# Kernel optimization log

Measured on AMD Instinct MI355X. Metric: run time of the kernel, lower is better.

Reference implementation:

```python
import jax, jax.numpy as jnp
import numpy as np

LAYERS = [3, 256, 256, 256, 256, 256, 256, 3]
W_BC, W_DIV, W_JXB = 1.0, 1.0, 1.0  # weight1 = [1.0, 1.0, 1.0]


def setup_inputs() -> dict:
    key = jax.random.key(0)
    ks = jax.random.split(key, 32)
    N0, NF = 16384, 32768
    inp = {
        "x0": jax.random.uniform(ks[0], (N0, 1), jnp.float32),
        "y0": jax.random.uniform(ks[1], (N0, 1), jnp.float32),
        "bx0": jax.random.normal(ks[2], (N0, 1), jnp.float32),
        "by0": jax.random.normal(ks[3], (N0, 1), jnp.float32),
        "bz0": jax.random.normal(ks[4], (N0, 1), jnp.float32),
        "xyz_f": jax.random.uniform(ks[5], (NF, 3), jnp.float32),
        "lb": jnp.zeros((3,), jnp.float32),
        "ub": jnp.ones((3,), jnp.float32),
    }
    # Xavier-normal weights, zero biases (as in initialize_NN)
    for l in range(len(LAYERS) - 1):
        fan_in, fan_out = LAYERS[l], LAYERS[l + 1]
        std = (2.0 / (fan_in + fan_out)) ** 0.5
        inp[f"W{l}"] = std * jax.random.normal(ks[6 + l], (fan_in, fan_out), jnp.float32)
        inp[f"b{l}"] = jnp.zeros((1, fan_out), jnp.float32)
    return inp


def reference(x0, y0, bx0, by0, bz0, xyz_f, lb, ub,
              W0, b0, W1, b1, W2, b2, W3, b3, W4, b4, W5, b5, W6, b6):
    Ws = [W0, W1, W2, W3, W4, W5, W6]
    bs = [b0, b1, b2, b3, b4, b5, b6]

    def net(p):  # p: (3,) -> (3,) field [bx, by, bz]
        h = 2.0 * (p - lb) / (ub - lb) - 1.0
        for W, b in zip(Ws[:-1], bs[:-1]):
            h = jnp.tanh(h @ W + b[0])
        return h @ Ws[-1] + bs[-1][0]

    # Boundary term at z = 0
    pts0 = jnp.concatenate([x0, y0, jnp.zeros_like(x0)], axis=1)  # (N0, 3)
    b_bc = jax.vmap(net)(pts0)  # (N0, 3)

    # One fused forward-mode pass gives the full 3x3 Jacobian + primal,
    # replacing the 9 separate autograd.grad sweeps of the torch code.
    def val_and_jac(p):
        primal, jac = jax.vmap(lambda t: jax.jvp(net, (p,), (t,)))(jnp.eye(3, dtype=p.dtype))
        return primal[0], jac  # jac[j, i] = d b_i / d x_j

    bf, jac = jax.vmap(val_and_jac)(xyz_f)  # (NF, 3), (NF, 3, 3)

    div = jac[:, 0, 0] + jac[:, 1, 1] + jac[:, 2, 2]  # bx_x + by_y + bz_z
    bx, by, bz = bf[:, 0], bf[:, 1], bf[:, 2]
    jx = jac[:, 1, 2] - jac[:, 2, 1]  # bz_y - by_z
    jy = jac[:, 2, 0] - jac[:, 0, 2]  # bx_z - bz_x
    jz = jac[:, 0, 1] - jac[:, 1, 0]  # by_x - bx_y
    jxb = (jy * bz - jz * by) ** 2 + (jz * bx - jx * bz) ** 2 + (jx * by - jy * bx) ** 2

    loss = (W_BC * jnp.mean((b_bc[:, 0:1] - bx0) ** 2)
            + W_BC * jnp.mean((b_bc[:, 1:2] - by0) ** 2)
            + W_BC * jnp.mean((b_bc[:, 2:3] - bz0) ** 2)
            + W_DIV * jnp.mean(div ** 2)
            + W_JXB * jnp.mean(jxb))
    return loss
```

## Files before the change

kernel.cpp:

```cpp
#include <hip/hip_runtime.h>
#include <math.h>

typedef short bf16x8 __attribute__((ext_vector_type(8)));
typedef float f32x4 __attribute__((ext_vector_type(4)));

#define NPT0 16384
#define NPTF 32768

__device__ __forceinline__ short f2b(float f) {
  union { float f; unsigned u; } v; v.f = f;
  return (short)((v.u + 0x7FFFu + ((v.u >> 16) & 1u)) >> 16);
}
__device__ __forceinline__ int cvtpk(float a, float b) {
  int r;
  asm("v_cvt_pk_bf16_f32 %0, %1, %2" : "=v"(r) : "v"(a), "v"(b));
  return r;
}
__device__ __forceinline__ float tanh_fast(float z) {
  const float e = __expf(2.f * z);
  return 1.f - 2.f * __builtin_amdgcn_rcpf(e + 1.f);
}
__device__ __forceinline__ int inplane(int n, int c) {
  return ((n >> 5) << 9) + ((((n >> 3) & 3) * 16 + c) << 3) + (n & 7);
}

__global__ void prep_kernel(const float* __restrict__ W1, const float* __restrict__ W2,
                            const float* __restrict__ W3, const float* __restrict__ W4,
                            const float* __restrict__ W5, const float* __restrict__ W6,
                            short* __restrict__ Wt)
{
  const int i = blockIdx.x * 256 + threadIdx.x;
  if (i < 5 * 65536) {
    const int layer = i >> 16;
    const float* src = layer == 0 ? W1 : layer == 1 ? W2 : layer == 2 ? W3
                     : layer == 3 ? W4 : W5;
    const int w  = i & 65535;
    const int nt = w >> 12;
    const int ks = (w >> 9) & 7;
    const int l  = (w >> 3) & 63;
    const int e  = w & 7;
    const int n  = nt * 16 + (l & 15);
    const int k  = ks * 32 + (l >> 4) * 8 + e;
    Wt[i] = f2b(src[k * 256 + n]);
  } else {
    const int w  = i - 5 * 65536;
    const int ks = w >> 9;
    const int l  = (w >> 3) & 63;
    const int e  = w & 7;
    const int n  = l & 15;
    const int k  = ks * 32 + (l >> 4) * 8 + e;
    Wt[i] = (n < 3) ? f2b(W6[k * 3 + n]) : (short)0;
  }
}

__global__ __launch_bounds__(512, 4) void field_kernel(
    const float* __restrict__ xyz_f,
    const float* __restrict__ lb, const float* __restrict__ ub,
    const float* __restrict__ W0, const float* __restrict__ b0,
    const float* __restrict__ b1, const float* __restrict__ b2,
    const float* __restrict__ b3, const float* __restrict__ b4,
    const float* __restrict__ b5,
    const short* __restrict__ Wt,
    const float* __restrict__ b6,
    float* __restrict__ part_div2, float* __restrict__ part_jxb)
{
  __shared__ short act[4 * 8192];
  __shared__ float redD[4 * 96];
  const int tid = threadIdx.x;
  const int lane = tid & 63;
  const int wv = tid >> 6;
  const int c = lane & 15;
  const int kg = lane >> 4;
  const int set = wv & 3;
  const int grp = wv >> 2;

  const float lbx = lb[0], lby = lb[1], lbz = lb[2];
  const float sx = 2.f / (ub[0] - lbx);
  const float sy = 2.f / (ub[1] - lby);
  const float sz = 2.f / (ub[2] - lbz);

  {
    const int pp = tid & 15;
    const int pg = (tid >> 4) & 1;
    const int pt = blockIdx.x * 32 + pg * 16 + pp;
    const int n0 = (tid >> 5) * 16;
    const float hx = (xyz_f[pt * 3 + 0] - lbx) * sx - 1.f;
    const float hy = (xyz_f[pt * 3 + 1] - lby) * sy - 1.f;
    const float hz = (xyz_f[pt * 3 + 2] - lbz) * sz - 1.f;
    float th[16], vx[16], vy[16], vz[16];
#pragma unroll
    for (int j = 0; j < 16; ++j) {
      const int n = n0 + j;
      const float w0 = W0[n], w1 = W0[256 + n], w2 = W0[512 + n];
      const float z = b0[n] + hx * w0 + hy * w1 + hz * w2;
      const float t = tanh_fast(z);
      const float g = 1.f - t * t;
      th[j] = t;
      vx[j] = g * sx * w0;
      vy[j] = g * sy * w1;
      vz[j] = g * sz * w2;
    }
    const int ks0 = n0 >> 5;
    const int kgb = (n0 >> 3) & 3;
#pragma unroll
    for (int half = 0; half < 2; ++half) {
      const int j0 = half * 8;
      const int idx = pg * 4096 + ks0 * 512 + ((kgb + half) * 16 + pp) * 8;
      int4 o0, o1, o2, o3;
      o0.x = cvtpk(th[j0+0], th[j0+1]); o0.y = cvtpk(th[j0+2], th[j0+3]);
      o0.z = cvtpk(th[j0+4], th[j0+5]); o0.w = cvtpk(th[j0+6], th[j0+7]);
      o1.x = cvtpk(vx[j0+0], vx[j0+1]); o1.y = cvtpk(vx[j0+2], vx[j0+3]);
      o1.z = cvtpk(vx[j0+4], vx[j0+5]); o1.w = cvtpk(vx[j0+6], vx[j0+7]);
      o2.x = cvtpk(vy[j0+0], vy[j0+1]); o2.y = cvtpk(vy[j0+2], vy[j0+3]);
      o2.z = cvtpk(vy[j0+4], vy[j0+5]); o2.w = cvtpk(vy[j0+6], vy[j0+7]);
      o3.x = cvtpk(vz[j0+0], vz[j0+1]); o3.y = cvtpk(vz[j0+2], vz[j0+3]);
      o3.z = cvtpk(vz[j0+4], vz[j0+5]); o3.w = cvtpk(vz[j0+6], vz[j0+7]);
      *(int4*)&act[idx]          = o0;
      *(int4*)&act[8192 + idx]   = o1;
      *(int4*)&act[16384 + idx]  = o2;
      *(int4*)&act[24576 + idx]  = o3;
    }
  }
  __syncthreads();

  const float* const bsArr[5] = {b1, b2, b3, b4, b5};

#pragma unroll
  for (int layer = 0; layer < 5; ++layer) {
    const short* wbase = Wt + layer * 65536 + (set * 4) * 4096 + lane * 8;

    f32x4 acc[4][4];
#pragma unroll
    for (int t = 0; t < 4; ++t)
#pragma unroll
      for (int s = 0; s < 4; ++s) acc[t][s] = (f32x4){0.f, 0.f, 0.f, 0.f};

#pragma unroll
    for (int ks = 0; ks < 8; ++ks) {
      const int sa = grp * 4096 + ks * 512 + lane * 8;
      const bf16x8 a0 = *(const bf16x8*)&act[sa];
      const bf16x8 a1 = *(const bf16x8*)&act[8192 + sa];
      const bf16x8 a2 = *(const bf16x8*)&act[16384 + sa];
      const bf16x8 a3 = *(const bf16x8*)&act[24576 + sa];
#pragma unroll
      for (int t = 0; t < 4; ++t) {
        const bf16x8 w = *(const bf16x8*)(wbase + t * 4096 + ks * 512);
        acc[t][0] = __builtin_amdgcn_mfma_f32_16x16x32_bf16(w, a0, acc[t][0], 0, 0, 0);
        acc[t][1] = __builtin_amdgcn_mfma_f32_16x16x32_bf16(w, a1, acc[t][1], 0, 0, 0);
        acc[t][2] = __builtin_amdgcn_mfma_f32_16x16x32_bf16(w, a2, acc[t][2], 0, 0, 0);
        acc[t][3] = __builtin_amdgcn_mfma_f32_16x16x32_bf16(w, a3, acc[t][3], 0, 0, 0);
      }
    }
    __syncthreads();

    const float* bl = bsArr[layer];
#pragma unroll
    for (int t = 0; t < 4; ++t) {
      const int n0 = (set * 4 + t) * 16 + kg * 4;
      const f32x4 bias = *(const f32x4*)(bl + n0);
      float th[4], gd[4];
#pragma unroll
      for (int r = 0; r < 4; ++r) {
        th[r] = tanh_fast(acc[t][0][r] + bias[r]);
        gd[r] = 1.f - th[r] * th[r];
      }
      int2 o0, o1, o2, o3;
      o0.x = cvtpk(th[0], th[1]);
      o0.y = cvtpk(th[2], th[3]);
      o1.x = cvtpk(gd[0] * acc[t][1][0], gd[1] * acc[t][1][1]);
      o1.y = cvtpk(gd[2] * acc[t][1][2], gd[3] * acc[t][1][3]);
      o2.x = cvtpk(gd[0] * acc[t][2][0], gd[1] * acc[t][2][1]);
      o2.y = cvtpk(gd[2] * acc[t][2][2], gd[3] * acc[t][2][3]);
      o3.x = cvtpk(gd[0] * acc[t][3][0], gd[1] * acc[t][3][1]);
      o3.y = cvtpk(gd[2] * acc[t][3][2], gd[3] * acc[t][3][3]);
      const int idx = grp * 4096 + inplane(n0, c);
      *(int2*)&act[idx]          = o0;
      *(int2*)&act[8192 + idx]   = o1;
      *(int2*)&act[16384 + idx]  = o2;
      *(int2*)&act[24576 + idx]  = o3;
    }
    __syncthreads();
  }

  {
    const int s = wv >> 1, g = wv & 1;
    const short* w6 = Wt + 5 * 65536 + lane * 8;
    f32x4 accT = (f32x4){0.f, 0.f, 0.f, 0.f};
#pragma unroll
    for (int ks = 0; ks < 8; ++ks) {
      const bf16x8 w = *(const bf16x8*)(w6 + ks * 512);
      const bf16x8 b = *(const bf16x8*)&act[s * 8192 + g * 4096 + ks * 512 + lane * 8];
      accT = __builtin_amdgcn_mfma_f32_16x16x32_bf16(w, b, accT, 0, 0, 0);
    }
    if (kg == 0) {
      redD[s * 96 + 0  + g * 16 + c] = accT[0];
      redD[s * 96 + 32 + g * 16 + c] = accT[1];
      redD[s * 96 + 64 + g * 16 + c] = accT[2];
    }
  }
  __syncthreads();
  if (tid < 32) {
    const int p = tid;
    const float bx = redD[0 + p]   + b6[0];
    const float by = redD[32 + p]  + b6[1];
    const float bz = redD[64 + p]  + b6[2];
    const float j00 = redD[96 + p],  j01 = redD[128 + p], j02 = redD[160 + p];
    const float j10 = redD[192 + p], j11 = redD[224 + p], j12 = redD[256 + p];
    const float j20 = redD[288 + p], j21 = redD[320 + p], j22 = redD[352 + p];
    const float dv = j00 + j11 + j22;
    const float jx = j12 - j21;
    const float jy = j20 - j02;
    const float jz = j01 - j10;
    const float e1 = jy * bz - jz * by;
    const float e2 = jz * bx - jx * bz;
    const float e3 = jx * by - jy * bx;
    float d2 = dv * dv;
    float jb = e1 * e1 + e2 * e2 + e3 * e3;
#pragma unroll
    for (int m = 1; m < 32; m <<= 1) {
      d2 += __shfl_xor(d2, m);
      jb += __shfl_xor(jb, m);
    }
    if (tid == 0) {
      part_div2[blockIdx.x] = d2;
      part_jxb[blockIdx.x]  = jb;
    }
  }
}

__global__ __launch_bounds__(512, 4) void bc_kernel(
    const float* __restrict__ x0, const float* __restrict__ y0,
    const float* __restrict__ bx0, const float* __restrict__ by0,
    const float* __restrict__ bz0,
    const float* __restrict__ lb, const float* __restrict__ ub,
    const float* __restrict__ W0, const float* __restrict__ b0,
    const float* __restrict__ b1, const float* __restrict__ b2,
    const float* __restrict__ b3, const float* __restrict__ b4,
    const float* __restrict__ b5,
    const short* __restrict__ Wt,
    const float* __restrict__ b6,
    float* __restrict__ part_bc)
{
  __shared__ short act[8192];
  __shared__ float red[2];
  const int tid = threadIdx.x;
  const int lane = tid & 63;
  const int wv = tid >> 6;
  const int c = lane & 15;
  const int kg = lane >> 4;

  const float lbx = lb[0], lby = lb[1], lbz = lb[2];
  const float sx = 2.f / (ub[0] - lbx);
  const float sy = 2.f / (ub[1] - lby);
  const float sz = 2.f / (ub[2] - lbz);

  {
    const int pp = tid & 15;
    const int pg = (tid >> 4) & 1;
    const int pt = blockIdx.x * 32 + pg * 16 + pp;
    const int n0 = (tid >> 5) * 16;
    const float hx = (x0[pt] - lbx) * sx - 1.f;
    const float hy = (y0[pt] - lby) * sy - 1.f;
    const float hz = (0.f - lbz) * sz - 1.f;
    float th[16];
#pragma unroll
    for (int j = 0; j < 16; ++j) {
      const int n = n0 + j;
      const float z = b0[n] + hx * W0[n] + hy * W0[256 + n] + hz * W0[512 + n];
      th[j] = tanh_fast(z);
    }
    const int ks0 = n0 >> 5;
    const int kgb = (n0 >> 3) & 3;
#pragma unroll
    for (int half = 0; half < 2; ++half) {
      const int j0 = half * 8;
      int4 o;
      o.x = cvtpk(th[j0+0], th[j0+1]); o.y = cvtpk(th[j0+2], th[j0+3]);
      o.z = cvtpk(th[j0+4], th[j0+5]); o.w = cvtpk(th[j0+6], th[j0+7]);
      *(int4*)&act[pg * 4096 + ks0 * 512 + ((kgb + half) * 16 + pp) * 8] = o;
    }
  }
  __syncthreads();

  const float* const bsArr[5] = {b1, b2, b3, b4, b5};

#pragma unroll
  for (int layer = 0; layer < 5; ++layer) {
    const short* wbase = Wt + layer * 65536 + (wv * 2) * 4096 + lane * 8;

    bf16x8 a[2][8];
#pragma unroll
    for (int g = 0; g < 2; ++g)
#pragma unroll
      for (int ks = 0; ks < 8; ++ks)
        a[g][ks] = *(const bf16x8*)&act[g * 4096 + ks * 512 + lane * 8];
    __syncthreads();

    f32x4 acc[2][2];
#pragma unroll
    for (int t = 0; t < 2; ++t)
#pragma unroll
      for (int g = 0; g < 2; ++g) acc[t][g] = (f32x4){0.f, 0.f, 0.f, 0.f};

#pragma unroll
    for (int ks = 0; ks < 8; ++ks) {
      const bf16x8 w0 = *(const bf16x8*)(wbase + ks * 512);
      const bf16x8 w1 = *(const bf16x8*)(wbase + 4096 + ks * 512);
      acc[0][0] = __builtin_amdgcn_mfma_f32_16x16x32_bf16(w0, a[0][ks], acc[0][0], 0, 0, 0);
      acc[0][1] = __builtin_amdgcn_mfma_f32_16x16x32_bf16(w0, a[1][ks], acc[0][1], 0, 0, 0);
      acc[1][0] = __builtin_amdgcn_mfma_f32_16x16x32_bf16(w1, a[0][ks], acc[1][0], 0, 0, 0);
      acc[1][1] = __builtin_amdgcn_mfma_f32_16x16x32_bf16(w1, a[1][ks], acc[1][1], 0, 0, 0);
    }

    const float* bl = bsArr[layer];
#pragma unroll
    for (int t = 0; t < 2; ++t) {
      const int n0 = (wv * 2 + t) * 16 + kg * 4;
      const f32x4 bias = *(const f32x4*)(bl + n0);
#pragma unroll
      for (int g = 0; g < 2; ++g) {
        float th[4];
#pragma unroll
        for (int r = 0; r < 4; ++r) th[r] = tanh_fast(acc[t][g][r] + bias[r]);
        int2 o;
        o.x = cvtpk(th[0], th[1]);
        o.y = cvtpk(th[2], th[3]);
        *(int2*)&act[g * 4096 + inplane(n0, c)] = o;
      }
    }
    __syncthreads();
  }

  if (wv < 2) {
    const int g = wv;
    const short* w6 = Wt + 5 * 65536 + lane * 8;
    f32x4 accT = (f32x4){0.f, 0.f, 0.f, 0.f};
#pragma unroll
    for (int ks = 0; ks < 8; ++ks) {
      const bf16x8 w = *(const bf16x8*)(w6 + ks * 512);
      const bf16x8 b = *(const bf16x8*)&act[g * 4096 + ks * 512 + lane * 8];
      accT = __builtin_amdgcn_mfma_f32_16x16x32_bf16(w, b, accT, 0, 0, 0);
    }
    if (lane < 16) {
      const int pt = blockIdx.x * 32 + g * 16 + lane;
      const float ex = accT[0] + b6[0] - bx0[pt];
      const float ey = accT[1] + b6[1] - by0[pt];
      const float ez = accT[2] + b6[2] - bz0[pt];
      float abc = ex * ex + ey * ey + ez * ez;
#pragma unroll
      for (int m = 1; m < 16; m <<= 1) abc += __shfl_xor(abc, m);
      if (lane == 0) red[g] = abc;
    }
  }
  __syncthreads();
  if (tid == 0) part_bc[blockIdx.x] = red[0] + red[1];
}

__global__ void reduce_kernel(const float* __restrict__ parts, float* __restrict__ out)
{
  __shared__ float sdata[12];
  const int tid = threadIdx.x, lane = tid & 63, wv = tid >> 6;
  float d = 0.f, j = 0.f, b = 0.f;
  for (int i = tid; i < 1024; i += 256) { d += parts[i]; j += parts[1024 + i]; }
  for (int i = tid; i < 512; i += 256) b += parts[2048 + i];
  for (int off = 32; off > 0; off >>= 1) {
    d += __shfl_down(d, off);
    j += __shfl_down(j, off);
    b += __shfl_down(b, off);
  }
  if (lane == 0) {
    sdata[wv * 3 + 0] = d;
    sdata[wv * 3 + 1] = j;
    sdata[wv * 3 + 2] = b;
  }
  __syncthreads();
  if (tid == 0) {
    float sd = 0.f, sj = 0.f, sb = 0.f;
    for (int w = 0; w < 4; ++w) {
      sd += sdata[w * 3 + 0];
      sj += sdata[w * 3 + 1];
      sb += sdata[w * 3 + 2];
    }
    out[0] = sb / (float)NPT0 + sd / (float)NPTF + sj / (float)NPTF;
  }
}

extern "C" void kernel_launch(void* const* d_in, const int* in_sizes, int n_in,
                              void* d_out, int out_size, void* d_ws, size_t ws_size,
                              hipStream_t stream)
{
  const float* x0    = (const float*)d_in[0];
  const float* y0    = (const float*)d_in[1];
  const float* bx0   = (const float*)d_in[2];
  const float* by0   = (const float*)d_in[3];
  const float* bz0   = (const float*)d_in[4];
  const float* xyz_f = (const float*)d_in[5];
  const float* lb    = (const float*)d_in[6];
  const float* ub    = (const float*)d_in[7];
  const float* W0 = (const float*)d_in[8];
  const float* b0 = (const float*)d_in[9];
  const float* W1 = (const float*)d_in[10];
  const float* b1 = (const float*)d_in[11];
  const float* W2 = (const float*)d_in[12];
  const float* b2 = (const float*)d_in[13];
  const float* W3 = (const float*)d_in[14];
  const float* b3 = (const float*)d_in[15];
  const float* W4 = (const float*)d_in[16];
  const float* b4 = (const float*)d_in[17];
  const float* W5 = (const float*)d_in[18];
  const float* b5 = (const float*)d_in[19];
  const float* W6 = (const float*)d_in[20];
  const float* b6 = (const float*)d_in[21];

  short* Wt = (short*)d_ws;
  float* parts = (float*)((char*)d_ws + (5 * 65536 + 4096) * sizeof(short));
  float* p_div2 = parts;
  float* p_jxb  = parts + 1024;
  float* p_bc   = parts + 2048;

  prep_kernel<<<1296, 256, 0, stream>>>(W1, W2, W3, W4, W5, W6, Wt);
  field_kernel<<<1024, 512, 0, stream>>>(xyz_f, lb, ub, W0, b0,
      b1, b2, b3, b4, b5, Wt, b6, p_div2, p_jxb);
  bc_kernel<<<512, 512, 0, stream>>>(x0, y0, bx0, by0, bz0, lb, ub, W0, b0,
      b1, b2, b3, b4, b5, Wt, b6, p_bc);
  reduce_kernel<<<1, 256, 0, stream>>>(parts, (float*)d_out);
}
```

Baseline: 127.0 us.

## Switch MLP matmuls from 16x16x32 to 32x32x16 MFMA tiles

Replaces the 16x16x32 bf16 MFMA tiling with 32x32x16 MFMA, changing the weight pre-pack layout, the shared-memory activation layout, and the wave-to-output-column split in both the field and boundary kernels. Each wave now owns 32 output neurons across all 32 points, so it issues one weight load per k-step instead of four. The aim is fewer instructions and weight fetches per FLOP, in exchange for larger accumulator register tiles and a repacked final layer whose padding grows from 16 to 32 columns.

```diff
diff --git a/kernel.cpp b/kernel.cpp
--- a/kernel.cpp
+++ b/kernel.cpp
@@ -3,6 +3,7 @@
 
 typedef short bf16x8 __attribute__((ext_vector_type(8)));
 typedef float f32x4 __attribute__((ext_vector_type(4)));
+typedef float f32x16 __attribute__((ext_vector_type(16)));
 
 #define NPT0 16384
 #define NPTF 32768
@@ -20,8 +21,8 @@
   const float e = __expf(2.f * z);
   return 1.f - 2.f * __builtin_amdgcn_rcpf(e + 1.f);
 }
-__device__ __forceinline__ int inplane(int n, int c) {
-  return ((n >> 5) << 9) + ((((n >> 3) & 3) * 16 + c) << 3) + (n & 7);
+__device__ __forceinline__ int inplane32(int k, int p) {
+  return ((k >> 4) << 9) + (((k >> 3) & 1) << 8) + (p << 3) + (k & 7);
 }
 
 __global__ void prep_kernel(const float* __restrict__ W1, const float* __restrict__ W2,
@@ -35,20 +36,20 @@
     const float* src = layer == 0 ? W1 : layer == 1 ? W2 : layer == 2 ? W3
                      : layer == 3 ? W4 : W5;
     const int w  = i & 65535;
-    const int nt = w >> 12;
-    const int ks = (w >> 9) & 7;
+    const int nt = w >> 13;
+    const int ks = (w >> 9) & 15;
     const int l  = (w >> 3) & 63;
     const int e  = w & 7;
-    const int n  = nt * 16 + (l & 15);
-    const int k  = ks * 32 + (l >> 4) * 8 + e;
+    const int n  = nt * 32 + (l & 31);
+    const int k  = ks * 16 + (l >> 5) * 8 + e;
     Wt[i] = f2b(src[k * 256 + n]);
   } else {
     const int w  = i - 5 * 65536;
     const int ks = w >> 9;
     const int l  = (w >> 3) & 63;
     const int e  = w & 7;
-    const int n  = l & 15;
-    const int k  = ks * 32 + (l >> 4) * 8 + e;
+    const int n  = l & 31;
+    const int k  = ks * 16 + (l >> 5) * 8 + e;
     Wt[i] = (n < 3) ? f2b(W6[k * 3 + n]) : (short)0;
   }
 }
@@ -69,10 +70,8 @@
   const int tid = threadIdx.x;
   const int lane = tid & 63;
   const int wv = tid >> 6;
-  const int c = lane & 15;
-  const int kg = lane >> 4;
-  const int set = wv & 3;
-  const int grp = wv >> 2;
+  const int p = lane & 31;
+  const int h = lane >> 5;
 
   const float lbx = lb[0], lby = lb[1], lbz = lb[2];
   const float sx = 2.f / (ub[0] - lbx);
@@ -80,9 +79,8 @@
   const float sz = 2.f / (ub[2] - lbz);
 
   {
-    const int pp = tid & 15;
-    const int pg = (tid >> 4) & 1;
-    const int pt = blockIdx.x * 32 + pg * 16 + pp;
+    const int pp = tid & 31;
+    const int pt = blockIdx.x * 32 + pp;
     const int n0 = (tid >> 5) * 16;
     const float hx = (xyz_f[pt * 3 + 0] - lbx) * sx - 1.f;
     const float hy = (xyz_f[pt * 3 + 1] - lby) * sy - 1.f;
@@ -100,12 +98,11 @@
       vy[j] = g * sy * w1;
       vz[j] = g * sz * w2;
     }
-    const int ks0 = n0 >> 5;
-    const int kgb = (n0 >> 3) & 3;
+    const int idx0 = (n0 >> 4) * 512 + pp * 8;
 #pragma unroll
     for (int half = 0; half < 2; ++half) {
       const int j0 = half * 8;
-      const int idx = pg * 4096 + ks0 * 512 + ((kgb + half) * 16 + pp) * 8;
+      const int idx = idx0 + half * 256;
       int4 o0, o1, o2, o3;
       o0.x = cvtpk(th[j0+0], th[j0+1]); o0.y = cvtpk(th[j0+2], th[j0+3]);
       o0.z = cvtpk(th[j0+4], th[j0+5]); o0.w = cvtpk(th[j0+6], th[j0+7]);
@@ -127,53 +124,50 @@
 
 #pragma unroll
   for (int layer = 0; layer < 5; ++layer) {
-    const short* wbase = Wt + layer * 65536 + (set * 4) * 4096 + lane * 8;
-
-    f32x4 acc[4][4];
-#pragma unroll
-    for (int t = 0; t < 4; ++t)
-#pragma unroll
-      for (int s = 0; s < 4; ++s) acc[t][s] = (f32x4){0.f, 0.f, 0.f, 0.f};
-
-#pragma unroll
-    for (int ks = 0; ks < 8; ++ks) {
-      const int sa = grp * 4096 + ks * 512 + lane * 8;
+    const short* wbase = Wt + layer * 65536 + wv * 8192 + lane * 8;
+
+    f32x16 acc[4];
+#pragma unroll
+    for (int s = 0; s < 4; ++s)
+#pragma unroll
+      for (int r = 0; r < 16; ++r) acc[s][r] = 0.f;
+
+#pragma unroll
+    for (int ks = 0; ks < 16; ++ks) {
+      const int sa = ks * 512 + lane * 8;
       const bf16x8 a0 = *(const bf16x8*)&act[sa];
       const bf16x8 a1 = *(const bf16x8*)&act[8192 + sa];
       const bf16x8 a2 = *(const bf16x8*)&act[16384 + sa];
       const bf16x8 a3 = *(const bf16x8*)&act[24576 + sa];
-#pragma unroll
-      for (int t = 0; t < 4; ++t) {
-        const bf16x8 w = *(const bf16x8*)(wbase + t * 4096 + ks * 512);
-        acc[t][0] = __builtin_amdgcn_mfma_f32_16x16x32_bf16(w, a0, acc[t][0], 0, 0, 0);
-        acc[t][1] = __builtin_amdgcn_mfma_f32_16x16x32_bf16(w, a1, acc[t][1], 0, 0, 0);
-        acc[t][2] = __builtin_amdgcn_mfma_f32_16x16x32_bf16(w, a2, acc[t][2], 0, 0, 0);
-        acc[t][3] = __builtin_amdgcn_mfma_f32_16x16x32_bf16(w, a3, acc[t][3], 0, 0, 0);
-      }
+      const bf16x8 w = *(const bf16x8*)(wbase + ks * 512);
+      acc[0] = __builtin_amdgcn_mfma_f32_32x32x16_bf16(w, a0, acc[0], 0, 0, 0);
+      acc[1] = __builtin_amdgcn_mfma_f32_32x32x16_bf16(w, a1, acc[1], 0, 0, 0);
+      acc[2] = __builtin_amdgcn_mfma_f32_32x32x16_bf16(w, a2, acc[2], 0, 0, 0);
+      acc[3] = __builtin_amdgcn_mfma_f32_32x32x16_bf16(w, a3, acc[3], 0, 0, 0);
     }
     __syncthreads();
 
     const float* bl = bsArr[layer];
 #pragma unroll
-    for (int t = 0; t < 4; ++t) {
-      const int n0 = (set * 4 + t) * 16 + kg * 4;
+    for (int q = 0; q < 4; ++q) {
+      const int n0 = wv * 32 + q * 8 + 4 * h;
       const f32x4 bias = *(const f32x4*)(bl + n0);
       float th[4], gd[4];
 #pragma unroll
       for (int r = 0; r < 4; ++r) {
-        th[r] = tanh_fast(acc[t][0][r] + bias[r]);
+        th[r] = tanh_fast(acc[0][q * 4 + r] + bias[r]);
         gd[r] = 1.f - th[r] * th[r];
       }
       int2 o0, o1, o2, o3;
       o0.x = cvtpk(th[0], th[1]);
       o0.y = cvtpk(th[2], th[3]);
-      o1.x = cvtpk(gd[0] * acc[t][1][0], gd[1] * acc[t][1][1]);
-      o1.y = cvtpk(gd[2] * acc[t][1][2], gd[3] * acc[t][1][3]);
-      o2.x = cvtpk(gd[0] * acc[t][2][0], gd[1] * acc[t][2][1]);
-      o2.y = cvtpk(gd[2] * acc[t][2][2], gd[3] * acc[t][2][3]);
-      o3.x = cvtpk(gd[0] * acc[t][3][0], gd[1] * acc[t][3][1]);
-      o3.y = cvtpk(gd[2] * acc[t][3][2], gd[3] * acc[t][3][3]);
-      const int idx = grp * 4096 + inplane(n0, c);
+      o1.x = cvtpk(gd[0] * acc[1][q*4+0], gd[1] * acc[1][q*4+1]);
+      o1.y = cvtpk(gd[2] * acc[1][q*4+2], gd[3] * acc[1][q*4+3]);
+      o2.x = cvtpk(gd[0] * acc[2][q*4+0], gd[1] * acc[2][q*4+1]);
+      o2.y = cvtpk(gd[2] * acc[2][q*4+2], gd[3] * acc[2][q*4+3]);
+      o3.x = cvtpk(gd[0] * acc[3][q*4+0], gd[1] * acc[3][q*4+1]);
+      o3.y = cvtpk(gd[2] * acc[3][q*4+2], gd[3] * acc[3][q*4+3]);
+      const int idx = inplane32(n0 & 255, p);
       *(int2*)&act[idx]          = o0;
       *(int2*)&act[8192 + idx]   = o1;
       *(int2*)&act[16384 + idx]  = o2;
@@ -182,31 +176,32 @@
     __syncthreads();
   }
 
-  {
-    const int s = wv >> 1, g = wv & 1;
+  if (wv < 4) {
     const short* w6 = Wt + 5 * 65536 + lane * 8;
-    f32x4 accT = (f32x4){0.f, 0.f, 0.f, 0.f};
-#pragma unroll
-    for (int ks = 0; ks < 8; ++ks) {
+    f32x16 accT;
+#pragma unroll
+    for (int r = 0; r < 16; ++r) accT[r] = 0.f;
+#pragma unroll
+    for (int ks = 0; ks < 16; ++ks) {
       const bf16x8 w = *(const bf16x8*)(w6 + ks * 512);
-      const bf16x8 b = *(const bf16x8*)&act[s * 8192 + g * 4096 + ks * 512 + lane * 8];
-      accT = __builtin_amdgcn_mfma_f32_16x16x32_bf16(w, b, accT, 0, 0, 0);
-    }
-    if (kg == 0) {
-      redD[s * 96 + 0  + g * 16 + c] = accT[0];
-      redD[s * 96 + 32 + g * 16 + c] = accT[1];
-      redD[s * 96 + 64 + g * 16 + c] = accT[2];
+      const bf16x8 b = *(const bf16x8*)&act[wv * 8192 + ks * 512 + lane * 8];
+      accT = __builtin_amdgcn_mfma_f32_32x32x16_bf16(w, b, accT, 0, 0, 0);
+    }
+    if (lane < 32) {
+      redD[wv * 96 + 0  + p] = accT[0];
+      redD[wv * 96 + 32 + p] = accT[1];
+      redD[wv * 96 + 64 + p] = accT[2];
     }
   }
   __syncthreads();
   if (tid < 32) {
-    const int p = tid;
-    const float bx = redD[0 + p]   + b6[0];
-    const float by = redD[32 + p]  + b6[1];
-    const float bz = redD[64 + p]  + b6[2];
-    const float j00 = redD[96 + p],  j01 = redD[128 + p], j02 = redD[160 + p];
-    const float j10 = redD[192 + p], j11 = redD[224 + p], j12 = redD[256 + p];
-    const float j20 = redD[288 + p], j21 = redD[320 + p], j22 = redD[352 + p];
+    const int pp = tid;
+    const float bx = redD[0 + pp]   + b6[0];
+    const float by = redD[32 + pp]  + b6[1];
+    const float bz = redD[64 + pp]  + b6[2];
+    const float j00 = redD[96 + pp],  j01 = redD[128 + pp], j02 = redD[160 + pp];
+    const float j10 = redD[192 + pp], j11 = redD[224 + pp], j12 = redD[256 + pp];
+    const float j20 = redD[288 + pp], j21 = redD[320 + pp], j22 = redD[352 + pp];
     const float dv = j00 + j11 + j22;
     const float jx = j12 - j21;
     const float jy = j20 - j02;
@@ -242,12 +237,11 @@
     float* __restrict__ part_bc)
 {
   __shared__ short act[8192];
-  __shared__ float red[2];
   const int tid = threadIdx.x;
   const int lane = tid & 63;
   const int wv = tid >> 6;
-  const int c = lane & 15;
-  const int kg = lane >> 4;
+  const int p = lane & 31;
+  const int h = lane >> 5;
 
   const float lbx = lb[0], lby = lb[1], lbz = lb[2];
   const float sx = 2.f / (ub[0] - lbx);
@@ -255,9 +249,8 @@
   const float sz = 2.f / (ub[2] - lbz);
 
   {
-    const int pp = tid & 15;
-    const int pg = (tid >> 4) & 1;
-    const int pt = blockIdx.x * 32 + pg * 16 + pp;
+    const int pp = tid & 31;
+    const int pt = blockIdx.x * 32 + pp;
     const int n0 = (tid >> 5) * 16;
     const float hx = (x0[pt] - lbx) * sx - 1.f;
     const float hy = (y0[pt] - lby) * sy - 1.f;
@@ -269,15 +262,14 @@
       const float z = b0[n] + hx * W0[n] + hy * W0[256 + n] + hz * W0[512 + n];
       th[j] = tanh_fast(z);
     }
-    const int ks0 = n0 >> 5;
-    const int kgb = (n0 >> 3) & 3;
+    const int idx0 = (n0 >> 4) * 512 + pp * 8;
 #pragma unroll
     for (int half = 0; half < 2; ++half) {
       const int j0 = half * 8;
       int4 o;
       o.x = cvtpk(th[j0+0], th[j0+1]); o.y = cvtpk(th[j0+2], th[j0+3]);
       o.z = cvtpk(th[j0+4], th[j0+5]); o.w = cvtpk(th[j0+6], th[j0+7]);
-      *(int4*)&act[pg * 4096 + ks0 * 512 + ((kgb + half) * 16 + pp) * 8] = o;
+      *(int4*)&act[idx0 + half * 256] = o;
     }
   }
   __syncthreads();
@@ -286,74 +278,55 @@
 
 #pragma unroll
   for (int layer = 0; layer < 5; ++layer) {
-    const short* wbase = Wt + layer * 65536 + (wv * 2) * 4096 + lane * 8;
-
-    bf16x8 a[2][8];
-#pragma unroll
-    for (int g = 0; g < 2; ++g)
-#pragma unroll
-      for (int ks = 0; ks < 8; ++ks)
-        a[g][ks] = *(const bf16x8*)&act[g * 4096 + ks * 512 + lane * 8];
+    const short* wbase = Wt + layer * 65536 + wv * 8192 + lane * 8;
+
+    f32x16 acc;
+#pragma unroll
+    for (int r = 0; r < 16; ++r) acc[r] = 0.f;
+
+#pragma unroll
+    for (int ks = 0; ks < 16; ++ks) {
+      const bf16x8 b = *(const bf16x8*)&act[ks * 512 + lane * 8];
+      const bf16x8 w = *(const bf16x8*)(wbase + ks * 512);
+      acc = __builtin_amdgcn_mfma_f32_32x32x16_bf16(w, b, acc, 0, 0, 0);
+    }
     __syncthreads();
 
-    f32x4 acc[2][2];
-#pragma unroll
-    for (int t = 0; t < 2; ++t)
-#pragma unroll
-      for (int g = 0; g < 2; ++g) acc[t][g] = (f32x4){0.f, 0.f, 0.f, 0.f};
-
-#pragma unroll
-    for (int ks = 0; ks < 8; ++ks) {
-      const bf16x8 w0 = *(const bf16x8*)(wbase + ks * 512);
-      const bf16x8 w1 = *(const bf16x8*)(wbase + 4096 + ks * 512);
-      acc[0][0] = __builtin_amdgcn_mfma_f32_16x16x32_bf16(w0, a[0][ks], acc[0][0], 0, 0, 0);
-      acc[0][1] = __builtin_amdgcn_mfma_f32_16x16x32_bf16(w0, a[1][ks], acc[0][1], 0, 0, 0);
-      acc[1][0] = __builtin_amdgcn_mfma_f32_16x16x32_bf16(w1, a[0][ks], acc[1][0], 0, 0, 0);
-      acc[1][1] = __builtin_amdgcn_mfma_f32_16x16x32_bf16(w1, a[1][ks], acc[1][1], 0, 0, 0);
-    }
-
     const float* bl = bsArr[layer];
 #pragma unroll
-    for (int t = 0; t < 2; ++t) {
-      const int n0 = (wv * 2 + t) * 16 + kg * 4;
+    for (int q = 0; q < 4; ++q) {
+      const int n0 = wv * 32 + q * 8 + 4 * h;
       const f32x4 bias = *(const f32x4*)(bl + n0);
-#pragma unroll
-      for (int g = 0; g < 2; ++g) {
-        float th[4];
-#pragma unroll
-        for (int r = 0; r < 4; ++r) th[r] = tanh_fast(acc[t][g][r] + bias[r]);
-        int2 o;
-        o.x = cvtpk(th[0], th[1]);
-        o.y = cvtpk(th[2], th[3]);
-        *(int2*)&act[g * 4096 + inplane(n0, c)] = o;
-      }
+      int2 o;
+      o.x = cvtpk(tanh_fast(acc[q*4+0] + bias[0]), tanh_fast(acc[q*4+1] + bias[1]));
+      o.y = cvtpk(tanh_fast(acc[q*4+2] + bias[2]), tanh_fast(acc[q*4+3] + bias[3]));
+      *(int2*)&act[inplane32(n0 & 255, p)] = o;
     }
     __syncthreads();
   }
 
-  if (wv < 2) {
-    const int g = wv;
+  if (wv == 0) {
     const short* w6 = Wt + 5 * 65536 + lane * 8;
-    f32x4 accT = (f32x4){0.f, 0.f, 0.f, 0.f};
-#pragma unroll
-    for (int ks = 0; ks < 8; ++ks) {
+    f32x16 accT;
+#pragma unroll
+    for (int r = 0; r < 16; ++r) accT[r] = 0.f;
+#pragma unroll
+    for (int ks = 0; ks < 16; ++ks) {
       const bf16x8 w = *(const bf16x8*)(w6 + ks * 512);
-      const bf16x8 b = *(const bf16x8*)&act[g * 4096 + ks * 512 + lane * 8];
-      accT = __builtin_amdgcn_mfma_f32_16x16x32_bf16(w, b, accT, 0, 0, 0);
-    }
-    if (lane < 16) {
-      const int pt = blockIdx.x * 32 + g * 16 + lane;
+      const bf16x8 b = *(const bf16x8*)&act[ks * 512 + lane * 8];
+      accT = __builtin_amdgcn_mfma_f32_32x32x16_bf16(w, b, accT, 0, 0, 0);
+    }
+    if (lane < 32) {
+      const int pt = blockIdx.x * 32 + p;
       const float ex = accT[0] + b6[0] - bx0[pt];
       const float ey = accT[1] + b6[1] - by0[pt];
       const float ez = accT[2] + b6[2] - bz0[pt];
       float abc = ex * ex + ey * ey + ez * ez;
 #pragma unroll
-      for (int m = 1; m < 16; m <<= 1) abc += __shfl_xor(abc, m);
-      if (lane == 0) red[g] = abc;
-    }
-  }
-  __syncthreads();
-  if (tid == 0) part_bc[blockIdx.x] = red[0] + red[1];
+      for (int m = 1; m < 32; m <<= 1) abc += __shfl_xor(abc, m);
+      if (lane == 0) part_bc[blockIdx.x] = abc;
+    }
+  }
 }
 
 __global__ void reduce_kernel(const float* __restrict__ parts, float* __restrict__ out)
@@ -413,12 +386,12 @@
   const float* b6 = (const float*)d_in[21];
 
   short* Wt = (short*)d_ws;
-  float* parts = (float*)((char*)d_ws + (5 * 65536 + 4096) * sizeof(short));
+  float* parts = (float*)((char*)d_ws + (5 * 65536 + 8192) * sizeof(short));
   float* p_div2 = parts;
   float* p_jxb  = parts + 1024;
   float* p_bc   = parts + 2048;
 
-  prep_kernel<<<1296, 256, 0, stream>>>(W1, W2, W3, W4, W5, W6, Wt);
+  prep_kernel<<<1312, 256, 0, stream>>>(W1, W2, W3, W4, W5, W6, Wt);
   field_kernel<<<1024, 512, 0, stream>>>(xyz_f, lb, ub, W0, b0,
       b1, b2, b3, b4, b5, Wt, b6, p_div2, p_jxb);
   bc_kernel<<<512, 512, 0, stream>>>(x0, y0, bx0, by0, bz0, lb, ub, W0, b0,
```

Result: faster. 111.7 us (-12.0%).
